# Kernel optimization log

Measured on AMD Instinct MI355X. Metric: run time of the kernel, lower is better.

Reference implementation:

```python
import jax, jax.numpy as jnp
import numpy as np

EPS_NORM = 1e-12   # torch F.normalize eps
EPS_BN = 1e-5      # BatchNorm1d eps
NEG_SLOPE = 0.01   # LeakyReLU default


def _l2_normalize(x, axis):
    # torch F.normalize: x / max(||x||, eps)
    n = jnp.sqrt(jnp.sum(x * x, axis=axis, keepdims=True))
    return x / jnp.maximum(n, EPS_NORM)


def setup_inputs() -> dict:
    key = jax.random.key(0)
    k1, k2, k3, k4, k5, k6, k7 = jax.random.split(key, 7)
    B, C, N, M, OUT = 8, 128, 4096, 4096, 128
    return {
        "input": jax.random.normal(k1, (B, C, N), dtype=jnp.float32),
        "target_g": jax.random.normal(k2, (B, C, M), dtype=jnp.float32),
        "weight": jax.random.normal(k3, (C, OUT), dtype=jnp.float32) * (1.0 / np.sqrt(OUT)),
        "gamma": jax.random.normal(k4, (OUT,), dtype=jnp.float32),
        "beta": jax.random.normal(k5, (OUT,), dtype=jnp.float32),
        "running_mean": jax.random.normal(k6, (OUT,), dtype=jnp.float32),
        "running_var": jax.random.uniform(k7, (OUT,), dtype=jnp.float32, minval=0.5, maxval=1.5),
    }


def reference(input, target_g, weight, gamma, beta, running_mean, running_var):
    # input: [B, C, N], target_g: [B, C, M]
    # cosine-similarity adjacency: [B, M, N]
    tg = _l2_normalize(target_g, axis=1)
    inp_n = _l2_normalize(input, axis=1)
    adj = jnp.einsum('bcm,bcn->bmn', tg, inp_n)
    adj = jax.nn.softmax(adj, axis=-1)
    # aggregate: [B, M, C]
    agg = jnp.einsum('bmn,bcn->bmc', adj, input)
    # project: [B, M, OUT] -> permute to [B, OUT, M]
    out = jnp.einsum('bmc,co->bom', agg, weight)
    # LeakyReLU then BatchNorm1d (eval mode, running stats)
    out = jnp.where(out >= 0, out, NEG_SLOPE * out)
    inv = jax.lax.rsqrt(running_var + EPS_BN)
    out = (out - running_mean[None, :, None]) * (inv * gamma)[None, :, None] + beta[None, :, None]
    return out
```

## Files before the change

kernel.cpp:

```cpp
#include <hip/hip_runtime.h>
#include <hip/hip_bf16.h>

#define BATCH 8
#define CDIM 128
#define NDIM 4096

typedef __bf16 bf16x8 __attribute__((ext_vector_type(8)));
typedef float f32x4 __attribute__((ext_vector_type(4)));
typedef float f32x16 __attribute__((ext_vector_type(16)));
typedef unsigned u32x4 __attribute__((ext_vector_type(4)));

#define QT_OFF 0u
#define KT_OFF 8388608u
#define VB_OFF 16777216u
#define WT_OFF 25165824u
#define SC_OFF (WT_OFF + 32768u)
#define BI_OFF (SC_OFF + 512u)

__device__ __forceinline__ f32x4 mfma16(bf16x8 a, bf16x8 b, f32x4 c) {
    return __builtin_amdgcn_mfma_f32_16x16x32_bf16(a, b, c, 0, 0, 0);
}
__device__ __forceinline__ f32x16 mfma32(bf16x8 a, bf16x8 b, f32x16 c) {
    return __builtin_amdgcn_mfma_f32_32x32x16_bf16(a, b, c, 0, 0, 0);
}

__device__ __forceinline__ unsigned pack2bf(float a, float b) {
    unsigned short ul = __builtin_bit_cast(unsigned short, (__bf16)a);
    unsigned short uh = __builtin_bit_cast(unsigned short, (__bf16)b);
    return (unsigned)ul | ((unsigned)uh << 16);
}

__device__ __forceinline__ void glds16(const void* g, void* l) {
    __builtin_amdgcn_global_load_lds((__attribute__((address_space(1))) void*)(void*)g,
                                     (__attribute__((address_space(3))) void*)l, 16, 0, 0);
}

__global__ __launch_bounds__(256) void prep_nt(const float* __restrict__ input,
                                               const float* __restrict__ tg,
                                               const float* __restrict__ wgt,
                                               const float* __restrict__ gamma,
                                               const float* __restrict__ beta,
                                               const float* __restrict__ mean,
                                               const float* __restrict__ var,
                                               void* __restrict__ ws) {
    __shared__ float Tt[64][129];
    __shared__ float psum[4][64];
    __shared__ float rn[64];
    const int n0 = blockIdx.x * 64;
    const int b  = blockIdx.y;
    const int tid = threadIdx.x;
    const float* src = (blockIdx.z == 0 ? input : tg) + (size_t)b * CDIM * NDIM;
    const float zscale = (blockIdx.z == 0) ? 1.0f : 1.44269504f;

    #pragma unroll
    for (int i = 0; i < 8; ++i) {
        int f = tid + i * 256;
        int c = f >> 4, j4 = f & 15;
        float4 v = *(const float4*)(src + (size_t)c * NDIM + n0 + j4 * 4);
        Tt[j4 * 4 + 0][c] = v.x;
        Tt[j4 * 4 + 1][c] = v.y;
        Tt[j4 * 4 + 2][c] = v.z;
        Tt[j4 * 4 + 3][c] = v.w;
    }
    __syncthreads();
    {
        int j = tid & 63, part = tid >> 6;
        float ss = 0.f;
        #pragma unroll 8
        for (int c = part * 32; c < part * 32 + 32; ++c) { float x = Tt[j][c]; ss += x * x; }
        psum[part][j] = ss;
    }
    __syncthreads();
    if (tid < 64) {
        float s = psum[0][tid] + psum[1][tid] + psum[2][tid] + psum[3][tid];
        rn[tid] = 1.0f / fmaxf(sqrtf(s), 1e-12f);
    }
    __syncthreads();

    __hip_bfloat16* dstT = (__hip_bfloat16*)((char*)ws + (blockIdx.z == 0 ? KT_OFF : QT_OFF))
                           + ((size_t)b * NDIM + n0) * CDIM;
    #pragma unroll
    for (int i = 0; i < 8; ++i) {
        int f = tid + i * 256;
        int j = f >> 5, c4 = f & 31;
        float r = rn[j] * zscale;
        float4 v = *(const float4*)&Tt[j][c4 * 4];
        uint2 pk; pk.x = pack2bf(v.x * r, v.y * r); pk.y = pack2bf(v.z * r, v.w * r);
        *(uint2*)((unsigned short*)dstT + (size_t)j * CDIM + c4 * 4) = pk;
    }
    if (blockIdx.z == 0) {
        __hip_bfloat16* vb = (__hip_bfloat16*)((char*)ws + VB_OFF) + (size_t)b * CDIM * NDIM + n0;
        #pragma unroll
        for (int i = 0; i < 8; ++i) {
            int f = tid + i * 256;
            int c = f >> 4, j4 = f & 15;
            float x0 = Tt[j4 * 4 + 0][c], x1 = Tt[j4 * 4 + 1][c];
            float x2 = Tt[j4 * 4 + 2][c], x3 = Tt[j4 * 4 + 3][c];
            uint2 pv; pv.x = pack2bf(x0, x1); pv.y = pack2bf(x2, x3);
            *(uint2*)((unsigned short*)vb + (size_t)c * NDIM + j4 * 4) = pv;
        }
    } else if (blockIdx.x == 0 && b == 0) {
        __hip_bfloat16* wT = (__hip_bfloat16*)((char*)ws + WT_OFF);
        float* sc = (float*)((char*)ws + SC_OFF);
        float* bi = (float*)((char*)ws + BI_OFF);
        #pragma unroll
        for (int i = 0; i < 64; ++i) {
            int f = tid + i * 256;
            int c = f >> 7, o = f & 127;
            wT[o * 128 + c] = __hip_bfloat16(wgt[c * 128 + o]);
        }
        if (tid < 128) {
            float inv = rsqrtf(var[tid] + 1e-5f);
            float s = inv * gamma[tid];
            sc[tid] = s;
            bi[tid] = beta[tid] - mean[tid] * s;
        }
    }
}

__global__ __launch_bounds__(512, 2) void flash6(const void* __restrict__ ws_,
                                                 float* __restrict__ out) {
    extern __shared__ char smem[];
    const char* ws = (const char*)ws_;
    const __hip_bfloat16* Qt = (const __hip_bfloat16*)(ws + QT_OFF);
    const __hip_bfloat16* Kt = (const __hip_bfloat16*)(ws + KT_OFF);
    const __hip_bfloat16* Vb = (const __hip_bfloat16*)(ws + VB_OFF);
    const __hip_bfloat16* wT = (const __hip_bfloat16*)(ws + WT_OFF);
    const float* scale = (const float*)(ws + SC_OFF);
    const float* bias  = (const float*)(ws + BI_OFF);

    const int bx = blockIdx.x;
    const int b  = bx & 7;
    const int m0 = (bx >> 3) * 128;
    const int tid = threadIdx.x;
    const int w = tid >> 6, lane = tid & 63;
    const int hf = lane >> 5;
    const int l31 = lane & 31;
    const int nt = w & 1;
    const int mt = w >> 1;

    const char* kgb = (const char*)(Kt + (size_t)b * NDIM * CDIM);
    const char* vgb = (const char*)(Vb + (size_t)b * CDIM * NDIM);

    bf16x8 qb[8];
    {
        const char* qrow = (const char*)Qt + ((size_t)b * NDIM + m0 + mt * 32 + l31) * 256 + hf * 16;
        #pragma unroll
        for (int s = 0; s < 8; ++s) qb[s] = *(const bf16x8*)(qrow + s * 32);
    }

    unsigned kOff[8];
    {
        int nn = nt * 32 + l31;
        #pragma unroll
        for (int s = 0; s < 8; ++s)
            kOff[s] = nn * 256 + (((2 * s + hf) ^ (nn & 15)) * 16);
    }
    unsigned vOff[2][4];
    #pragma unroll
    for (int t = 0; t < 2; ++t)
        #pragma unroll
        for (int ca = 0; ca < 4; ++ca) {
            int c = ca * 32 + l31;
            vOff[t][ca] = 32768 + c * 256 + (((nt * 4 + t * 2 + hf) ^ (c & 15)) * 16);
        }

    const int t4 = tid >> 4, j16 = tid & 15;
    const int swz = j16 ^ (t4 & 15);
    const char* kSrcP = kgb + t4 * 256 + swz * 16;
    const char* vSrcP = vgb + (size_t)t4 * 8192 + swz * 16;
    const unsigned kDstB = w * 1024;
    const unsigned vDstB = 32768 + w * 1024;

    f32x16 oacc[4];
    #pragma unroll
    for (int ca = 0; ca < 4; ++ca)
        #pragma unroll
        for (int i = 0; i < 16; ++i) oacc[ca][i] = 0.f;
    float lacc = 0.f;

    #pragma unroll
    for (int i = 0; i < 4; ++i) glds16(kSrcP + i * 8192, smem + kDstB + i * 8192);
    #pragma unroll
    for (int i = 0; i < 4; ++i) glds16(vSrcP + (size_t)i * 262144, smem + vDstB + i * 8192);
    kSrcP += 32768; vSrcP += 256;

    auto make_pf = [&](const f32x16& st, bf16x8 pf[2]) {
        unsigned d[8];
        float lsum = 0.f;
        #pragma unroll
        for (int rq = 0; rq < 4; ++rq) {
            float e0 = exp2f(st[rq * 4 + 0]);
            float e1 = exp2f(st[rq * 4 + 1]);
            float e2 = exp2f(st[rq * 4 + 2]);
            float e3 = exp2f(st[rq * 4 + 3]);
            lsum += (e0 + e1) + (e2 + e3);
            d[rq * 2 + 0] = pack2bf(e0, e1);
            d[rq * 2 + 1] = pack2bf(e2, e3);
        }
        lacc += lsum;
        unsigned o[8];
        #pragma unroll
        for (int j = 0; j < 8; ++j) o[j] = (unsigned)__shfl_xor((int)d[j], 32, 64);
        #pragma unroll
        for (int t = 0; t < 2; ++t) {
            u32x4 tv;
            tv.x = hf ? o[4 * t + 2] : d[4 * t + 0];
            tv.y = hf ? o[4 * t + 3] : d[4 * t + 1];
            tv.z = hf ? d[4 * t + 2] : o[4 * t + 0];
            tv.w = hf ? d[4 * t + 3] : o[4 * t + 1];
            pf[t] = __builtin_bit_cast(bf16x8, tv);
        }
    };

    auto body = [&](const unsigned bo, const bool do_pref) {
        asm volatile("s_waitcnt vmcnt(0) lgkmcnt(0)\ns_barrier" ::: "memory");
        if (do_pref) {
            const unsigned obo = bo ^ 65536u;
            #pragma unroll
            for (int i = 0; i < 4; ++i)
                glds16(kSrcP + i * 8192, smem + obo + kDstB + i * 8192);
            #pragma unroll
            for (int i = 0; i < 4; ++i)
                glds16(vSrcP + (size_t)i * 262144, smem + obo + vDstB + i * 8192);
            kSrcP += 32768; vSrcP += 256;
        }

        f32x16 st0, st1;
        #pragma unroll
        for (int i = 0; i < 16; ++i) { st0[i] = 0.f; st1[i] = 0.f; }
        #pragma unroll
        for (int s = 0; s < 8; ++s) {
            bf16x8 kf = *(const bf16x8*)(smem + bo + kOff[s]);
            st0 = mfma32(kf, qb[s], st0);
        }
        #pragma unroll
        for (int s = 0; s < 8; ++s) {
            bf16x8 kf = *(const bf16x8*)(smem + bo + 16384 + kOff[s]);
            st1 = mfma32(kf, qb[s], st1);
        }

        bf16x8 pf0[2];
        make_pf(st0, pf0);
        #pragma unroll
        for (int t = 0; t < 2; ++t)
            #pragma unroll
            for (int ca = 0; ca < 4; ++ca) {
                bf16x8 vf = *(const bf16x8*)(smem + bo + vOff[t][ca]);
                oacc[ca] = mfma32(vf, pf0[t], oacc[ca]);
            }

        bf16x8 pf1[2];
        make_pf(st1, pf1);
        #pragma unroll
        for (int t = 0; t < 2; ++t)
            #pragma unroll
            for (int ca = 0; ca < 4; ++ca) {
                bf16x8 vf = *(const bf16x8*)(smem + bo + (vOff[t][ca] ^ 128u));
                oacc[ca] = mfma32(vf, pf1[t], oacc[ca]);
            }
    };

    for (int ii = 0; ii < 16; ++ii) {
        body(0u, true);
        body(65536u, ii != 15);
    }

    float lw = lacc + __shfl_xor(lacc, 32, 64);
    __syncthreads();
    char* slab = smem + mt * 16512;
    if (nt == 1) {
        float4* dst = (float4*)slab;
        #pragma unroll
        for (int ca = 0; ca < 4; ++ca)
            #pragma unroll
            for (int rq = 0; rq < 4; ++rq) {
                float4 t = { oacc[ca][rq * 4 + 0], oacc[ca][rq * 4 + 1],
                             oacc[ca][rq * 4 + 2], oacc[ca][rq * 4 + 3] };
                dst[(ca * 4 + rq) * 64 + lane] = t;
            }
        if (lane < 32) ((float*)(slab + 16384))[l31] = lw;
    }
    __syncthreads();
    char* sAgg = smem + 66560;
    if (nt == 0) {
        float linv = 1.0f / (lw + ((const float*)(slab + 16384))[l31]);
        const float4* srcp = (const float4*)slab;
        int m = mt * 32 + l31;
        char* aggRow = sAgg + m * 256;
        const int mx = (m & 7) << 1;
        #pragma unroll
        for (int ca = 0; ca < 4; ++ca)
            #pragma unroll
            for (int rq = 0; rq < 4; ++rq) {
                float4 ov = srcp[(ca * 4 + rq) * 64 + lane];
                float v0 = (oacc[ca][rq * 4 + 0] + ov.x) * linv;
                float v1 = (oacc[ca][rq * 4 + 1] + ov.y) * linv;
                float v2 = (oacc[ca][rq * 4 + 2] + ov.z) * linv;
                float v3 = (oacc[ca][rq * 4 + 3] + ov.w) * linv;
                int cq = ca * 8 + rq * 2 + hf;
                uint2 pk; pk.x = pack2bf(v0, v1); pk.y = pack2bf(v2, v3);
                *(uint2*)(aggRow + ((cq ^ mx) * 8)) = pk;
            }
    }
    __syncthreads();

    const int li = lane & 15, q = lane >> 4;
    const int pm = w * 16 + li;
    f32x4 racc[8];
    #pragma unroll
    for (int ob = 0; ob < 8; ++ob) { racc[ob][0]=0.f; racc[ob][1]=0.f; racc[ob][2]=0.f; racc[ob][3]=0.f; }
    #pragma unroll
    for (int ks = 0; ks < 4; ++ks) {
        int slot8 = ((ks * 4 + q) * 2) ^ ((li & 7) << 1);
        bf16x8 af = *(const bf16x8*)(sAgg + pm * 256 + slot8 * 8);
        #pragma unroll
        for (int ob = 0; ob < 8; ++ob) {
            bf16x8 wf = *(const bf16x8*)((const char*)wT + (ob * 16 + li) * 256 + ks * 64 + q * 16);
            racc[ob] = mfma16(af, wf, racc[ob]);
        }
    }

    float* outb = out + (size_t)b * CDIM * NDIM + m0 + w * 16;
    #pragma unroll
    for (int ob = 0; ob < 8; ++ob) {
        int o = ob * 16 + li;
        float sc = scale[o], bi = bias[o];
        float4 vst;
        float v0 = racc[ob][0]; v0 = (v0 >= 0.f) ? v0 : 0.01f * v0; vst.x = v0 * sc + bi;
        float v1 = racc[ob][1]; v1 = (v1 >= 0.f) ? v1 : 0.01f * v1; vst.y = v1 * sc + bi;
        float v2 = racc[ob][2]; v2 = (v2 >= 0.f) ? v2 : 0.01f * v2; vst.z = v2 * sc + bi;
        float v3 = racc[ob][3]; v3 = (v3 >= 0.f) ? v3 : 0.01f * v3; vst.w = v3 * sc + bi;
        *(float4*)(outb + (size_t)o * NDIM + q * 4) = vst;
    }
}

extern "C" void kernel_launch(void* const* d_in, const int* in_sizes, int n_in,
                              void* d_out, int out_size, void* d_ws, size_t ws_size,
                              hipStream_t stream) {
    const float* input  = (const float*)d_in[0];
    const float* tg     = (const float*)d_in[1];
    const float* weight = (const float*)d_in[2];
    const float* gamma  = (const float*)d_in[3];
    const float* beta   = (const float*)d_in[4];
    const float* rmean  = (const float*)d_in[5];
    const float* rvar   = (const float*)d_in[6];
    float* out = (float*)d_out;

    (void)in_sizes; (void)n_in; (void)out_size; (void)ws_size;

    hipFuncSetAttribute(reinterpret_cast<const void*>(flash6),
                        hipFuncAttributeMaxDynamicSharedMemorySize, 131072);

    dim3 gprep(NDIM / 64, BATCH, 2);
    prep_nt<<<gprep, 256, 0, stream>>>(input, tg, weight, gamma, beta, rmean, rvar, d_ws);
    flash6<<<dim3(256), 512, 131072, stream>>>(d_ws, out);
}
```

Measured before the change: 195.4 us.

## Pre-swizzle K/V into MFMA fragment layout and load directly to registers

The prep kernel now writes K and V in bf16 in the exact per-lane MFMA fragment order, so the attention kernel can read fragments straight from global memory into registers instead of staging tiles through LDS with global_load_lds and barriers. The main loop is restructured into register double-buffered steps of 32 columns, prefetching the next K fragment set and the current V fragments before the compute. This removes the LDS round-trip, the per-tile barriers and the LDS reads. In exchange each of the 8 waves fetches its own copy of K/V fragments from global/L2, raising global traffic, and register pressure increases. LDS allocation is also reduced.

```diff
diff --git a/kernel.cpp b/kernel.cpp
--- a/kernel.cpp
+++ b/kernel.cpp
@@ -28,11 +28,6 @@
     unsigned short ul = __builtin_bit_cast(unsigned short, (__bf16)a);
     unsigned short uh = __builtin_bit_cast(unsigned short, (__bf16)b);
     return (unsigned)ul | ((unsigned)uh << 16);
-}
-
-__device__ __forceinline__ void glds16(const void* g, void* l) {
-    __builtin_amdgcn_global_load_lds((__attribute__((address_space(1))) void*)(void*)g,
-                                     (__attribute__((address_space(3))) void*)l, 16, 0, 0);
 }
 
 __global__ __launch_bounds__(256) void prep_nt(const float* __restrict__ input,
@@ -50,7 +45,6 @@
     const int b  = blockIdx.y;
     const int tid = threadIdx.x;
     const float* src = (blockIdx.z == 0 ? input : tg) + (size_t)b * CDIM * NDIM;
-    const float zscale = (blockIdx.z == 0) ? 1.0f : 1.44269504f;
 
     #pragma unroll
     for (int i = 0; i < 8; ++i) {
@@ -77,54 +71,70 @@
     }
     __syncthreads();
 
-    __hip_bfloat16* dstT = (__hip_bfloat16*)((char*)ws + (blockIdx.z == 0 ? KT_OFF : QT_OFF))
-                           + ((size_t)b * NDIM + n0) * CDIM;
-    #pragma unroll
-    for (int i = 0; i < 8; ++i) {
-        int f = tid + i * 256;
-        int j = f >> 5, c4 = f & 31;
-        float r = rn[j] * zscale;
-        float4 v = *(const float4*)&Tt[j][c4 * 4];
-        uint2 pk; pk.x = pack2bf(v.x * r, v.y * r); pk.y = pack2bf(v.z * r, v.w * r);
-        *(uint2*)((unsigned short*)dstT + (size_t)j * CDIM + c4 * 4) = pk;
-    }
     if (blockIdx.z == 0) {
-        __hip_bfloat16* vb = (__hip_bfloat16*)((char*)ws + VB_OFF) + (size_t)b * CDIM * NDIM + n0;
+        char* kfb = (char*)ws + KT_OFF + (size_t)b * 1048576u + (size_t)blockIdx.x * 16384u;
+        char* vfb = (char*)ws + VB_OFF + (size_t)b * 1048576u + (size_t)blockIdx.x * 16384u;
+        #pragma unroll
+        for (int i = 0; i < 4; ++i) {
+            int q = tid + i * 256;
+            int lane = q & 63, l31 = q & 31, hf = (q >> 5) & 1;
+            int s = (q >> 6) & 7, ntk = q >> 9;
+            int nl = ntk * 32 + l31;
+            float r = rn[nl];
+            int c0 = s * 16 + hf * 8;
+            uint4 pk;
+            pk.x = pack2bf(Tt[nl][c0 + 0] * r, Tt[nl][c0 + 1] * r);
+            pk.y = pack2bf(Tt[nl][c0 + 2] * r, Tt[nl][c0 + 3] * r);
+            pk.z = pack2bf(Tt[nl][c0 + 4] * r, Tt[nl][c0 + 5] * r);
+            pk.w = pack2bf(Tt[nl][c0 + 6] * r, Tt[nl][c0 + 7] * r);
+            *(uint4*)(kfb + ntk * 8192 + s * 1024 + lane * 16) = pk;
+            int tt = (q >> 6) & 1, ca = (q >> 7) & 3, ntv = q >> 9;
+            int c = ca * 32 + l31;
+            int nv = ntv * 32 + tt * 16 + hf * 8;
+            uint4 pv;
+            pv.x = pack2bf(Tt[nv + 0][c], Tt[nv + 1][c]);
+            pv.y = pack2bf(Tt[nv + 2][c], Tt[nv + 3][c]);
+            pv.z = pack2bf(Tt[nv + 4][c], Tt[nv + 5][c]);
+            pv.w = pack2bf(Tt[nv + 6][c], Tt[nv + 7][c]);
+            *(uint4*)(vfb + ntv * 8192 + (ca * 2 + tt) * 1024 + lane * 16) = pv;
+        }
+    } else {
+        __hip_bfloat16* dstT = (__hip_bfloat16*)((char*)ws + QT_OFF)
+                               + ((size_t)b * NDIM + n0) * CDIM;
         #pragma unroll
         for (int i = 0; i < 8; ++i) {
             int f = tid + i * 256;
-            int c = f >> 4, j4 = f & 15;
-            float x0 = Tt[j4 * 4 + 0][c], x1 = Tt[j4 * 4 + 1][c];
-            float x2 = Tt[j4 * 4 + 2][c], x3 = Tt[j4 * 4 + 3][c];
-            uint2 pv; pv.x = pack2bf(x0, x1); pv.y = pack2bf(x2, x3);
-            *(uint2*)((unsigned short*)vb + (size_t)c * NDIM + j4 * 4) = pv;
-        }
-    } else if (blockIdx.x == 0 && b == 0) {
-        __hip_bfloat16* wT = (__hip_bfloat16*)((char*)ws + WT_OFF);
-        float* sc = (float*)((char*)ws + SC_OFF);
-        float* bi = (float*)((char*)ws + BI_OFF);
-        #pragma unroll
-        for (int i = 0; i < 64; ++i) {
-            int f = tid + i * 256;
-            int c = f >> 7, o = f & 127;
-            wT[o * 128 + c] = __hip_bfloat16(wgt[c * 128 + o]);
-        }
-        if (tid < 128) {
-            float inv = rsqrtf(var[tid] + 1e-5f);
-            float s = inv * gamma[tid];
-            sc[tid] = s;
-            bi[tid] = beta[tid] - mean[tid] * s;
-        }
-    }
-}
-
-__global__ __launch_bounds__(512, 2) void flash6(const void* __restrict__ ws_,
+            int j = f >> 5, c4 = f & 31;
+            float r = rn[j] * 1.44269504f;
+            float4 v = *(const float4*)&Tt[j][c4 * 4];
+            uint2 pk; pk.x = pack2bf(v.x * r, v.y * r); pk.y = pack2bf(v.z * r, v.w * r);
+            *(uint2*)((unsigned short*)dstT + (size_t)j * CDIM + c4 * 4) = pk;
+        }
+        if (blockIdx.x == 0 && b == 0) {
+            __hip_bfloat16* wT = (__hip_bfloat16*)((char*)ws + WT_OFF);
+            float* sc = (float*)((char*)ws + SC_OFF);
+            float* bi = (float*)((char*)ws + BI_OFF);
+            #pragma unroll
+            for (int i = 0; i < 64; ++i) {
+                int f = tid + i * 256;
+                int c = f >> 7, o = f & 127;
+                wT[o * 128 + c] = __hip_bfloat16(wgt[c * 128 + o]);
+            }
+            if (tid < 128) {
+                float inv = rsqrtf(var[tid] + 1e-5f);
+                float s = inv * gamma[tid];
+                sc[tid] = s;
+                bi[tid] = beta[tid] - mean[tid] * s;
+            }
+        }
+    }
+}
+
+__global__ __launch_bounds__(512, 2) void flash7(const void* __restrict__ ws_,
                                                  float* __restrict__ out) {
     extern __shared__ char smem[];
     const char* ws = (const char*)ws_;
     const __hip_bfloat16* Qt = (const __hip_bfloat16*)(ws + QT_OFF);
-    const __hip_bfloat16* Kt = (const __hip_bfloat16*)(ws + KT_OFF);
-    const __hip_bfloat16* Vb = (const __hip_bfloat16*)(ws + VB_OFF);
     const __hip_bfloat16* wT = (const __hip_bfloat16*)(ws + WT_OFF);
     const float* scale = (const float*)(ws + SC_OFF);
     const float* bias  = (const float*)(ws + BI_OFF);
@@ -139,9 +149,6 @@
     const int nt = w & 1;
     const int mt = w >> 1;
 
-    const char* kgb = (const char*)(Kt + (size_t)b * NDIM * CDIM);
-    const char* vgb = (const char*)(Vb + (size_t)b * CDIM * NDIM);
-
     bf16x8 qb[8];
     {
         const char* qrow = (const char*)Qt + ((size_t)b * NDIM + m0 + mt * 32 + l31) * 256 + hf * 16;
@@ -149,28 +156,8 @@
         for (int s = 0; s < 8; ++s) qb[s] = *(const bf16x8*)(qrow + s * 32);
     }
 
-    unsigned kOff[8];
-    {
-        int nn = nt * 32 + l31;
-        #pragma unroll
-        for (int s = 0; s < 8; ++s)
-            kOff[s] = nn * 256 + (((2 * s + hf) ^ (nn & 15)) * 16);
-    }
-    unsigned vOff[2][4];
-    #pragma unroll
-    for (int t = 0; t < 2; ++t)
-        #pragma unroll
-        for (int ca = 0; ca < 4; ++ca) {
-            int c = ca * 32 + l31;
-            vOff[t][ca] = 32768 + c * 256 + (((nt * 4 + t * 2 + hf) ^ (c & 15)) * 16);
-        }
-
-    const int t4 = tid >> 4, j16 = tid & 15;
-    const int swz = j16 ^ (t4 & 15);
-    const char* kSrcP = kgb + t4 * 256 + swz * 16;
-    const char* vSrcP = vgb + (size_t)t4 * 8192 + swz * 16;
-    const unsigned kDstB = w * 1024;
-    const unsigned vDstB = 32768 + w * 1024;
+    const char* kp = ws + KT_OFF + (size_t)b * 1048576u + nt * 8192 + lane * 16;
+    const char* vp = ws + VB_OFF + (size_t)b * 1048576u + nt * 8192 + lane * 16;
 
     f32x16 oacc[4];
     #pragma unroll
@@ -178,12 +165,6 @@
         #pragma unroll
         for (int i = 0; i < 16; ++i) oacc[ca][i] = 0.f;
     float lacc = 0.f;
-
-    #pragma unroll
-    for (int i = 0; i < 4; ++i) glds16(kSrcP + i * 8192, smem + kDstB + i * 8192);
-    #pragma unroll
-    for (int i = 0; i < 4; ++i) glds16(vSrcP + (size_t)i * 262144, smem + vDstB + i * 8192);
-    kSrcP += 32768; vSrcP += 256;
 
     auto make_pf = [&](const f32x16& st, bf16x8 pf[2]) {
         unsigned d[8];
@@ -213,57 +194,39 @@
         }
     };
 
-    auto body = [&](const unsigned bo, const bool do_pref) {
-        asm volatile("s_waitcnt vmcnt(0) lgkmcnt(0)\ns_barrier" ::: "memory");
-        if (do_pref) {
-            const unsigned obo = bo ^ 65536u;
-            #pragma unroll
-            for (int i = 0; i < 4; ++i)
-                glds16(kSrcP + i * 8192, smem + obo + kDstB + i * 8192);
-            #pragma unroll
-            for (int i = 0; i < 4; ++i)
-                glds16(vSrcP + (size_t)i * 262144, smem + obo + vDstB + i * 8192);
-            kSrcP += 32768; vSrcP += 256;
-        }
-
-        f32x16 st0, st1;
-        #pragma unroll
-        for (int i = 0; i < 16; ++i) { st0[i] = 0.f; st1[i] = 0.f; }
-        #pragma unroll
-        for (int s = 0; s < 8; ++s) {
-            bf16x8 kf = *(const bf16x8*)(smem + bo + kOff[s]);
-            st0 = mfma32(kf, qb[s], st0);
-        }
-        #pragma unroll
-        for (int s = 0; s < 8; ++s) {
-            bf16x8 kf = *(const bf16x8*)(smem + bo + 16384 + kOff[s]);
-            st1 = mfma32(kf, qb[s], st1);
-        }
-
-        bf16x8 pf0[2];
-        make_pf(st0, pf0);
-        #pragma unroll
-        for (int t = 0; t < 2; ++t)
-            #pragma unroll
-            for (int ca = 0; ca < 4; ++ca) {
-                bf16x8 vf = *(const bf16x8*)(smem + bo + vOff[t][ca]);
-                oacc[ca] = mfma32(vf, pf0[t], oacc[ca]);
-            }
-
-        bf16x8 pf1[2];
-        make_pf(st1, pf1);
-        #pragma unroll
-        for (int t = 0; t < 2; ++t)
-            #pragma unroll
-            for (int ca = 0; ca < 4; ++ca) {
-                bf16x8 vf = *(const bf16x8*)(smem + bo + (vOff[t][ca] ^ 128u));
-                oacc[ca] = mfma32(vf, pf1[t], oacc[ca]);
-            }
+    bf16x8 kA[8], kB[8];
+    #pragma unroll
+    for (int s = 0; s < 8; ++s) kA[s] = *(const bf16x8*)(kp + s * 1024);
+    kp += 16384;
+
+    auto step = [&](bf16x8* kc, bf16x8* kn) {
+        bf16x8 vf[8];
+        #pragma unroll
+        for (int u = 0; u < 8; ++u) vf[u] = *(const bf16x8*)(vp + u * 1024);
+        vp += 16384;
+        #pragma unroll
+        for (int s = 0; s < 8; ++s) kn[s] = *(const bf16x8*)(kp + s * 1024);
+        kp += 16384;
+
+        f32x16 st;
+        #pragma unroll
+        for (int i = 0; i < 16; ++i) st[i] = 0.f;
+        #pragma unroll
+        for (int s = 0; s < 8; ++s) st = mfma32(kc[s], qb[s], st);
+
+        bf16x8 pf[2];
+        make_pf(st, pf);
+
+        #pragma unroll
+        for (int ca = 0; ca < 4; ++ca) {
+            oacc[ca] = mfma32(vf[ca * 2 + 0], pf[0], oacc[ca]);
+            oacc[ca] = mfma32(vf[ca * 2 + 1], pf[1], oacc[ca]);
+        }
     };
 
-    for (int ii = 0; ii < 16; ++ii) {
-        body(0u, true);
-        body(65536u, ii != 15);
+    for (int it = 0; it < 32; ++it) {
+        step(kA, kB);
+        step(kB, kA);
     }
 
     float lw = lacc + __shfl_xor(lacc, 32, 64);
@@ -349,10 +312,10 @@
 
     (void)in_sizes; (void)n_in; (void)out_size; (void)ws_size;
 
-    hipFuncSetAttribute(reinterpret_cast<const void*>(flash6),
-                        hipFuncAttributeMaxDynamicSharedMemorySize, 131072);
+    hipFuncSetAttribute(reinterpret_cast<const void*>(flash7),
+                        hipFuncAttributeMaxDynamicSharedMemorySize, 99328);
 
     dim3 gprep(NDIM / 64, BATCH, 2);
     prep_nt<<<gprep, 256, 0, stream>>>(input, tg, weight, gamma, beta, rmean, rvar, d_ws);
-    flash6<<<dim3(256), 512, 131072, stream>>>(d_ws, out);
-}
+    flash7<<<dim3(256), 512, 99328, stream>>>(d_ws, out);
+}
```

After: 270.7 us. 38.5% more time.
